# Optimization experiments

Measured on AMD Instinct MI355X. Metric: run time of the kernel, lower is better.

Reference implementation:

```python
import jax, jax.numpy as jnp
import numpy as np

INT8_MAX = 127.0

def _quant_ste(x, axis):
    """Dynamic symmetric int8 fake-quant along `axis` (per-channel scales).
    Returns dequantized values; math matches int8 dot * scales (AQT-style)."""
    amax = jnp.max(jnp.abs(x), axis=axis, keepdims=True)
    scale = jnp.maximum(amax, 1e-6) / INT8_MAX
    q = jnp.clip(jnp.round(x / scale), -INT8_MAX, INT8_MAX)
    return q * scale

def setup_inputs() -> dict:
    key = jax.random.key(0)
    k1, k2 = jax.random.split(key)
    inputs = jax.random.normal(k1, (4, 2048, 4096), dtype=jnp.float32)
    kernel = jax.random.normal(k2, (4096, 4096), dtype=jnp.float32) * 0.02
    return {"inputs": inputs, "kernel": kernel}

def reference(inputs, kernel):
    # eqn: '...y,yz->...z' with quantized dot_general:
    # per-row (last-axis) dynamic int8 quant of activations,
    # per-output-column int8 quant of kernel, int8 matmul, dequant by scales.
    xq = _quant_ste(inputs, axis=-1)   # [B, S, D]
    kq = _quant_ste(kernel, axis=0)    # [D, F]
    return jnp.einsum('bsd,df->bsf', xq, kq)  # [B, S, F]
```

## Files before the change

### kernel.cpp

```cpp
#include <hip/hip_runtime.h>


#define M_DIM 8192
#define K_DIM 4096
#define N_DIM 4096

typedef int v4i __attribute__((ext_vector_type(4)));
typedef __attribute__((address_space(3))) void lds_void_t;
typedef const __attribute__((address_space(1))) void g_void_t;

__global__ void quant_act(const float* __restrict__ X,
                          signed char* __restrict__ At,
                          float* __restrict__ sx) {
  const int row = blockIdx.x;
  const int t = threadIdx.x;
  const float* xr = X + (size_t)row * K_DIM;
  float4 v[4];
  float am = 0.f;
#pragma unroll
  for (int c = 0; c < 4; ++c) {
    v[c] = ((const float4*)xr)[c * 256 + t];
    am = fmaxf(am, fmaxf(fmaxf(fabsf(v[c].x), fabsf(v[c].y)),
                         fmaxf(fabsf(v[c].z), fabsf(v[c].w))));
  }
#pragma unroll
  for (int off = 32; off > 0; off >>= 1)
    am = fmaxf(am, __shfl_down(am, off));
  __shared__ float red[4];
  __shared__ float s_inv;
  __shared__ unsigned int shuf[1024];
  if ((t & 63) == 0) red[t >> 6] = am;
  __syncthreads();
  if (t == 0) {
    float m = fmaxf(fmaxf(red[0], red[1]), fmaxf(red[2], red[3]));
    float scale = fmaxf(m, 1e-6f) / 127.0f;
    sx[row] = scale;
    s_inv = 1.0f / scale;
  }
  __syncthreads();
  const float inv = s_inv;
#pragma unroll
  for (int c = 0; c < 4; ++c) {
    int q0 = (int)fminf(fmaxf(rintf(v[c].x * inv), -127.f), 127.f);
    int q1 = (int)fminf(fmaxf(rintf(v[c].y * inv), -127.f), 127.f);
    int q2 = (int)fminf(fmaxf(rintf(v[c].z * inv), -127.f), 127.f);
    int q3 = (int)fminf(fmaxf(rintf(v[c].w * inv), -127.f), 127.f);
    shuf[c * 256 + t] = (q0 & 255) | ((q1 & 255) << 8) | ((q2 & 255) << 16) | (q3 << 24);
  }
  __syncthreads();
  v4i w = *(const v4i*)&shuf[t * 4];
  signed char* dst = At + (size_t)(row >> 4) * 65536 + t * 256 + (row & 15) * 16;
  *(v4i*)dst = w;
}

__global__ void wk_amax_part(const float* __restrict__ Kmat, float* __restrict__ part) {
  const int f = blockIdx.x * 256 + threadIdx.x;
  const float* p = Kmat + (size_t)(blockIdx.y * 128) * N_DIM + f;
  float a0 = 0.f, a1 = 0.f, a2 = 0.f, a3 = 0.f;
#pragma unroll 4
  for (int i = 0; i < 32; ++i) {
    a0 = fmaxf(a0, fabsf(p[0 * N_DIM]));
    a1 = fmaxf(a1, fabsf(p[1 * N_DIM]));
    a2 = fmaxf(a2, fabsf(p[2 * N_DIM]));
    a3 = fmaxf(a3, fabsf(p[3 * N_DIM]));
    p += 4 * N_DIM;
  }
  part[(size_t)blockIdx.y * N_DIM + f] = fmaxf(fmaxf(a0, a1), fmaxf(a2, a3));
}

__global__ void wk_amax_comb(const float* __restrict__ part,
                             float* __restrict__ sk, float* __restrict__ skinv) {
  const int f = blockIdx.x * 256 + threadIdx.x;
  float am = 0.f;
#pragma unroll
  for (int s = 0; s < 32; ++s) am = fmaxf(am, part[(size_t)s * N_DIM + f]);
  float scale = fmaxf(am, 1e-6f) / 127.0f;
  sk[f] = scale;
  skinv[f] = 1.0f / scale;
}

__global__ void wk_quant(const float* __restrict__ Kmat,
                         const float* __restrict__ skinv,
                         signed char* __restrict__ Bt) {
  const int f0 = (blockIdx.x & 63) * 64;
  const int d0 = (blockIdx.x >> 6) * 64;
  const int t = threadIdx.x;
  const int fl = t & 63;
  const int dl0 = t >> 6;
  __shared__ __align__(16) signed char tile[64 * 80];
  const float inv = skinv[f0 + fl];
#pragma unroll
  for (int c = 0; c < 16; ++c) {
    const int dl = c * 4 + dl0;
    float vv = Kmat[(size_t)(d0 + dl) * N_DIM + f0 + fl];
    float q = fminf(fmaxf(rintf(vv * inv), -127.f), 127.f);
    tile[fl * 80 + dl] = (signed char)(int)q;
  }
  __syncthreads();
  const int frow = t >> 2;
  const int ksl = t & 3;
  v4i w = *(const v4i*)&tile[frow * 80 + ksl * 16];
  const int f = f0 + frow;
  signed char* dst = Bt + (size_t)(f >> 4) * 65536 + ((d0 >> 4) + ksl) * 256 + (f & 15) * 16;
  *(v4i*)dst = w;
}

__global__ __launch_bounds__(256, 2) void gemm_i8(
    const signed char* __restrict__ At, const signed char* __restrict__ Bt,
    const float* __restrict__ sx, const float* __restrict__ sk,
    float* __restrict__ C) {
  const int n0 = blockIdx.x * 128;
  const int m0 = blockIdx.y * 128;
  const int t = threadIdx.x;
  const int lane = t & 63;
  const int wave = t >> 6;
  const int wm = (wave >> 1) * 64;
  const int wn = (wave & 1) * 64;
  const int lrow = lane & 15;
  const int lq = lane >> 4;

  __shared__ __align__(16) signed char lds[32768];
  signed char* lA = lds;
  signed char* lB = lds + 16384;

  v4i acc[4][4];
#pragma unroll
  for (int i = 0; i < 4; ++i)
#pragma unroll
    for (int j = 0; j < 4; ++j) acc[i][j] = (v4i){0, 0, 0, 0};

  const signed char* Abase = At + (size_t)(m0 >> 4) * 65536;
  const signed char* Bbase = Bt + (size_t)(n0 >> 4) * 65536;

  const int la = ((wave >> 1) * 4) * 2048 + lane * 16;
  const int lb = ((wave & 1) * 4) * 2048 + lane * 16;

  for (int kb = 0; kb < K_DIM; kb += 128) {
    const int kofs = kb * 16;
#pragma unroll
    for (int j = 0; j < 4; ++j) {
      const int c = j * 256 + t;
      const int mt_i = c >> 7;
      const int inner = c & 127;
      __builtin_amdgcn_global_load_lds(
          (g_void_t*)(Abase + (size_t)mt_i * 65536 + kofs + inner * 16),
          (lds_void_t*)(lA + c * 16), 16, 0, 0);
      __builtin_amdgcn_global_load_lds(
          (g_void_t*)(Bbase + (size_t)mt_i * 65536 + kofs + inner * 16),
          (lds_void_t*)(lB + c * 16), 16, 0, 0);
    }
    __syncthreads();
#pragma unroll
    for (int s = 0; s < 2; ++s) {
      v4i af[4], bf[4];
#pragma unroll
      for (int i = 0; i < 4; ++i) af[i] = *(const v4i*)(lA + la + i * 2048 + s * 1024);
#pragma unroll
      for (int i = 0; i < 4; ++i) bf[i] = *(const v4i*)(lB + lb + i * 2048 + s * 1024);
#pragma unroll
      for (int mi = 0; mi < 4; ++mi)
#pragma unroll
        for (int ni = 0; ni < 4; ++ni)
          acc[mi][ni] =
              __builtin_amdgcn_mfma_i32_16x16x64_i8(af[mi], bf[ni], acc[mi][ni], 0, 0, 0);
    }
    __syncthreads();
  }

#pragma unroll
  for (int mi = 0; mi < 4; ++mi) {
#pragma unroll
    for (int ni = 0; ni < 4; ++ni) {
      const int gn = n0 + wn + ni * 16 + lrow;
      const float skv = sk[gn];
#pragma unroll
      for (int r = 0; r < 4; ++r) {
        const int gm = m0 + wm + mi * 16 + lq * 4 + r;
        C[(size_t)gm * N_DIM + gn] = (float)acc[mi][ni][r] * sx[gm] * skv;
      }
    }
  }
}

extern "C" void kernel_launch(void* const* d_in, const int* in_sizes, int n_in,
                              void* d_out, int out_size, void* d_ws, size_t ws_size,
                              hipStream_t stream) {
  const float* X = (const float*)d_in[0];
  const float* W = (const float*)d_in[1];
  float* out = (float*)d_out;
  char* ws = (char*)d_ws;

  signed char* At = (signed char*)ws;
  signed char* Bt = (signed char*)(ws + 33554432);
  float* sx = (float*)(ws + 50331648);
  float* sk = (float*)(ws + 50364416);
  float* skinv = (float*)(ws + 50380800);
  float* part = (float*)(ws + 50397184);

  quant_act<<<M_DIM, 256, 0, stream>>>(X, At, sx);
  wk_amax_part<<<dim3(16, 32), 256, 0, stream>>>(W, part);
  wk_amax_comb<<<16, 256, 0, stream>>>(part, sk, skinv);
  wk_quant<<<4096, 256, 0, stream>>>(W, skinv, Bt);
  gemm_i8<<<dim3(N_DIM / 128, M_DIM / 128), 256, 0, stream>>>(At, Bt, sx, sk, out);
}
```

Before: 419.1 us.

## Switch GEMM to 32x32x32 int8 MFMA with 32-row tiled operand layout

The GEMM now uses the 32x32x32 int8 MFMA instruction (2x2 per wave) in place of 4x4 tiles of 16x16x64, which cuts LDS fragment reads per MFMA. The pre-packed A and B layouts change from 16-row to 32-row tiles so they match the new fragment shape, and both quant kernels write the new layout. The activation quant kernel also handles one row per wave (4 rows per block) with a wave-level xor-shuffle reduction, dropping the block-wide syncs for the scale. The epilogue remaps accumulator registers to the 32x32 output layout, and the scattered stores may coalesce differently.

```diff
diff --git a/kernel.cpp b/kernel.cpp
--- a/kernel.cpp
+++ b/kernel.cpp
@@ -6,51 +6,56 @@
 #define N_DIM 4096
 
 typedef int v4i __attribute__((ext_vector_type(4)));
+typedef int v16i __attribute__((ext_vector_type(16)));
 typedef __attribute__((address_space(3))) void lds_void_t;
 typedef const __attribute__((address_space(1))) void g_void_t;
 
 __global__ void quant_act(const float* __restrict__ X,
                           signed char* __restrict__ At,
                           float* __restrict__ sx) {
-  const int row = blockIdx.x;
+  const int row0 = blockIdx.x * 4;
   const int t = threadIdx.x;
+  const int lane = t & 63;
+  const int w = t >> 6;
+  const int row = row0 + w;
   const float* xr = X + (size_t)row * K_DIM;
-  float4 v[4];
+
+  float4 v[16];
   float am = 0.f;
 #pragma unroll
-  for (int c = 0; c < 4; ++c) {
-    v[c] = ((const float4*)xr)[c * 256 + t];
+  for (int c = 0; c < 16; ++c) {
+    v[c] = ((const float4*)xr)[c * 64 + lane];
     am = fmaxf(am, fmaxf(fmaxf(fabsf(v[c].x), fabsf(v[c].y)),
                          fmaxf(fabsf(v[c].z), fabsf(v[c].w))));
   }
 #pragma unroll
   for (int off = 32; off > 0; off >>= 1)
-    am = fmaxf(am, __shfl_down(am, off));
-  __shared__ float red[4];
-  __shared__ float s_inv;
-  __shared__ unsigned int shuf[1024];
-  if ((t & 63) == 0) red[t >> 6] = am;
-  __syncthreads();
-  if (t == 0) {
-    float m = fmaxf(fmaxf(red[0], red[1]), fmaxf(red[2], red[3]));
-    float scale = fmaxf(m, 1e-6f) / 127.0f;
-    sx[row] = scale;
-    s_inv = 1.0f / scale;
-  }
-  __syncthreads();
-  const float inv = s_inv;
-#pragma unroll
-  for (int c = 0; c < 4; ++c) {
+    am = fmaxf(am, __shfl_xor(am, off));
+  const float scale = fmaxf(am, 1e-6f) / 127.0f;
+  if (lane == 0) sx[row] = scale;
+  const float inv = 1.0f / scale;
+
+  __shared__ unsigned int shuf[4096];
+#pragma unroll
+  for (int c = 0; c < 16; ++c) {
     int q0 = (int)fminf(fmaxf(rintf(v[c].x * inv), -127.f), 127.f);
     int q1 = (int)fminf(fmaxf(rintf(v[c].y * inv), -127.f), 127.f);
     int q2 = (int)fminf(fmaxf(rintf(v[c].z * inv), -127.f), 127.f);
     int q3 = (int)fminf(fmaxf(rintf(v[c].w * inv), -127.f), 127.f);
-    shuf[c * 256 + t] = (q0 & 255) | ((q1 & 255) << 8) | ((q2 & 255) << 16) | (q3 << 24);
+    shuf[w * 1024 + c * 64 + lane] =
+        (q0 & 255) | ((q1 & 255) << 8) | ((q2 & 255) << 16) | (q3 << 24);
   }
   __syncthreads();
-  v4i w = *(const v4i*)&shuf[t * 4];
-  signed char* dst = At + (size_t)(row >> 4) * 65536 + t * 256 + (row & 15) * 16;
-  *(v4i*)dst = w;
+  const size_t tbase = (size_t)(row0 >> 5) * 131072;
+  const int rbase = row0 & 31;
+#pragma unroll
+  for (int i = 0; i < 4; ++i) {
+    const int c = i * 256 + t;
+    const int ks = c >> 2;
+    const int r4 = c & 3;
+    v4i val = *(const v4i*)&shuf[r4 * 1024 + ks * 4];
+    *(v4i*)(At + tbase + ks * 512 + (rbase + r4) * 16) = val;
+  }
 }
 
 __global__ void wk_amax_part(const float* __restrict__ Kmat, float* __restrict__ part) {
@@ -101,7 +106,8 @@
   const int ksl = t & 3;
   v4i w = *(const v4i*)&tile[frow * 80 + ksl * 16];
   const int f = f0 + frow;
-  signed char* dst = Bt + (size_t)(f >> 4) * 65536 + ((d0 >> 4) + ksl) * 256 + (f & 15) * 16;
+  signed char* dst =
+      Bt + (size_t)(f >> 5) * 131072 + ((d0 >> 4) + ksl) * 512 + (f & 31) * 16;
   *(v4i*)dst = w;
 }
 
@@ -116,66 +122,69 @@
   const int wave = t >> 6;
   const int wm = (wave >> 1) * 64;
   const int wn = (wave & 1) * 64;
-  const int lrow = lane & 15;
-  const int lq = lane >> 4;
 
   __shared__ __align__(16) signed char lds[32768];
   signed char* lA = lds;
   signed char* lB = lds + 16384;
 
-  v4i acc[4][4];
-#pragma unroll
-  for (int i = 0; i < 4; ++i)
-#pragma unroll
-    for (int j = 0; j < 4; ++j) acc[i][j] = (v4i){0, 0, 0, 0};
-
-  const signed char* Abase = At + (size_t)(m0 >> 4) * 65536;
-  const signed char* Bbase = Bt + (size_t)(n0 >> 4) * 65536;
-
-  const int la = ((wave >> 1) * 4) * 2048 + lane * 16;
-  const int lb = ((wave & 1) * 4) * 2048 + lane * 16;
+  v16i acc[2][2];
+#pragma unroll
+  for (int i = 0; i < 2; ++i)
+#pragma unroll
+    for (int j = 0; j < 2; ++j)
+#pragma unroll
+      for (int e = 0; e < 16; ++e) acc[i][j][e] = 0;
+
+  const signed char* Abase = At + (size_t)(m0 >> 5) * 131072;
+  const signed char* Bbase = Bt + (size_t)(n0 >> 5) * 131072;
+
+  const int la = (wave >> 1) * 2 * 4096 + lane * 16;
+  const int lb = (wave & 1) * 2 * 4096 + lane * 16;
 
   for (int kb = 0; kb < K_DIM; kb += 128) {
-    const int kofs = kb * 16;
+    const int kofs = kb * 32;
 #pragma unroll
     for (int j = 0; j < 4; ++j) {
       const int c = j * 256 + t;
-      const int mt_i = c >> 7;
-      const int inner = c & 127;
+      const int tl = c >> 8;
+      const int inner = c & 255;
       __builtin_amdgcn_global_load_lds(
-          (g_void_t*)(Abase + (size_t)mt_i * 65536 + kofs + inner * 16),
+          (g_void_t*)(Abase + (size_t)tl * 131072 + kofs + inner * 16),
           (lds_void_t*)(lA + c * 16), 16, 0, 0);
       __builtin_amdgcn_global_load_lds(
-          (g_void_t*)(Bbase + (size_t)mt_i * 65536 + kofs + inner * 16),
+          (g_void_t*)(Bbase + (size_t)tl * 131072 + kofs + inner * 16),
           (lds_void_t*)(lB + c * 16), 16, 0, 0);
     }
     __syncthreads();
 #pragma unroll
-    for (int s = 0; s < 2; ++s) {
-      v4i af[4], bf[4];
-#pragma unroll
-      for (int i = 0; i < 4; ++i) af[i] = *(const v4i*)(lA + la + i * 2048 + s * 1024);
-#pragma unroll
-      for (int i = 0; i < 4; ++i) bf[i] = *(const v4i*)(lB + lb + i * 2048 + s * 1024);
-#pragma unroll
-      for (int mi = 0; mi < 4; ++mi)
-#pragma unroll
-        for (int ni = 0; ni < 4; ++ni)
+    for (int s = 0; s < 4; ++s) {
+      v4i af[2], bf[2];
+#pragma unroll
+      for (int i = 0; i < 2; ++i) af[i] = *(const v4i*)(lA + la + i * 4096 + s * 1024);
+#pragma unroll
+      for (int i = 0; i < 2; ++i) bf[i] = *(const v4i*)(lB + lb + i * 4096 + s * 1024);
+#pragma unroll
+      for (int mi = 0; mi < 2; ++mi)
+#pragma unroll
+        for (int ni = 0; ni < 2; ++ni)
           acc[mi][ni] =
-              __builtin_amdgcn_mfma_i32_16x16x64_i8(af[mi], bf[ni], acc[mi][ni], 0, 0, 0);
+              __builtin_amdgcn_mfma_i32_32x32x32_i8(af[mi], bf[ni], acc[mi][ni], 0, 0, 0);
     }
     __syncthreads();
   }
 
-#pragma unroll
-  for (int mi = 0; mi < 4; ++mi) {
-#pragma unroll
-    for (int ni = 0; ni < 4; ++ni) {
-      const int gn = n0 + wn + ni * 16 + lrow;
+  const int lcol = lane & 31;
+  const int lhi = (lane >> 5) * 4;
+#pragma unroll
+  for (int mi = 0; mi < 2; ++mi) {
+#pragma unroll
+    for (int ni = 0; ni < 2; ++ni) {
+      const int gn = n0 + wn + ni * 32 + lcol;
       const float skv = sk[gn];
 #pragma unroll
-      for (int r = 0; r < 4; ++r) {
-        const int gm = m0 + wm + mi * 16 + lq * 4 + r;
+      for (int r = 0; r < 16; ++r) {
+        const int rowl = (r & 3) + 8 * (r >> 2) + lhi;
+        const int gm = m0 + wm + mi * 32 + rowl;
         C[(size_t)gm * N_DIM + gn] = (float)acc[mi][ni][r] * sx[gm] * skv;
       }
     }
@@ -197,7 +206,7 @@
   float* skinv = (float*)(ws + 50380800);
   float* part = (float*)(ws + 50397184);
 
-  quant_act<<<M_DIM, 256, 0, stream>>>(X, At, sx);
+  quant_act<<<M_DIM / 4, 256, 0, stream>>>(X, At, sx);
   wk_amax_part<<<dim3(16, 32), 256, 0, stream>>>(W, part);
   wk_amax_comb<<<16, 256, 0, stream>>>(part, sk, skinv);
   wk_quant<<<4096, 256, 0, stream>>>(W, skinv, Bt);
```

Result: no change. 427.1 us (+1.9%).
